# Performance work log

Measured on AMD Instinct MI355X. Metric: run time of the kernel, lower is better.

The kernel has to match this reference:

```python
import jax, jax.numpy as jnp
import numpy as np

HIDDEN = 2048
GAMMA = 0.96875
SCALE_BASE = 512  # XPOS default from torchscale / Jamie-Stirling/RetNet


def _xpos(x, downscale=False):
    # x: [B, L, d]. Faithful port of XPOS with offset=0.
    B, L, d = x.shape
    half = d // 2
    # per-dim scale vector: (arange(0,d,2) + 0.4d) / (1.4d)
    scale_vec = (jnp.arange(0, d, 2, dtype=jnp.float32) + 0.4 * d) / (1.4 * d)  # [half]
    power = jnp.arange(L, dtype=jnp.float32) / SCALE_BASE                        # [L]
    scale = scale_vec[None, :] ** power[:, None]                                 # [L, half]
    # fixed_pos_embedding over `half` frequency dims
    inv_freq = 1.0 / (10000.0 ** (jnp.arange(half, dtype=jnp.float32) / half))   # [half]
    sinusoid = jnp.arange(L, dtype=jnp.float32)[:, None] * inv_freq[None, :]     # [L, half]
    sin, cos = jnp.sin(sinusoid), jnp.cos(sinusoid)
    if downscale:
        scale = 1.0 / scale
    # duplicate_interleave: [L, half] -> [L, d] with each column repeated twice
    sin_s = jnp.repeat(sin * scale, 2, axis=-1)  # [L, d]
    cos_s = jnp.repeat(cos * scale, 2, axis=-1)  # [L, d]
    # rotate_every_two
    x1 = x[..., 0::2]
    x2 = x[..., 1::2]
    rot = jnp.stack((-x2, x1), axis=-1).reshape(x.shape)
    return x * cos_s[None] + rot * sin_s[None]


def _decay_matrix(L):
    n = jnp.arange(L)[:, None]
    m = jnp.arange(L)[None, :]
    mask = n >= m
    # clamp exponent to avoid overflow where masked (torch sets NaN->0)
    D = jnp.where(mask, GAMMA ** jnp.maximum(n - m, 0).astype(jnp.float32), 0.0)
    return D  # [L, L]


def setup_inputs() -> dict:
    key = jax.random.key(0)
    kx, kq, kk, kv = jax.random.split(key, 4)
    B, S, H = 4, 2048, HIDDEN
    X = jax.random.normal(kx, (B, S, H), dtype=jnp.float32)
    W_Q = jax.random.normal(kq, (H, H), dtype=jnp.float32) / H
    W_K = jax.random.normal(kk, (H, H), dtype=jnp.float32) / H
    W_V = jax.random.normal(kv, (H, H), dtype=jnp.float32) / H
    return {"X": X, "W_Q": W_Q, "W_K": W_K, "W_V": W_V}


def reference(X, W_Q, W_K, W_V):
    B, S, H = X.shape
    Q = _xpos(X @ W_Q)                   # [B, S, H]
    K = _xpos(X @ W_K, downscale=True)   # [B, S, H]
    V = X @ W_V                          # [B, S, H]
    D = _decay_matrix(S)                 # [S, S]
    att = jnp.einsum("bnh,bmh->bnm", Q, K) * D[None]  # [B, S, S]
    return att @ V                       # [B, S, H]
```

## Files before the change

kernel.cpp:

```cpp
#include <hip/hip_runtime.h>
#include <math.h>


typedef __attribute__((ext_vector_type(8))) short short8;
typedef __attribute__((ext_vector_type(4))) float f32x4;
typedef __attribute__((ext_vector_type(4))) unsigned short us4;

#define BM 128
#define ABAND 384

static __device__ __forceinline__ unsigned short f2bf(float f) {
    unsigned int u = __float_as_uint(f);
    u += 0x7FFFu + ((u >> 16) & 1u);
    return (unsigned short)(u >> 16);
}

static __device__ __forceinline__ void gload16(const unsigned short* g, unsigned short* l) {
    __builtin_amdgcn_global_load_lds(
        (const __attribute__((address_space(1))) unsigned int*)g,
        (__attribute__((address_space(3))) unsigned int*)l, 16, 0, 0);
}

template <int STAGE, int BNt, int BKt>
static __device__ __forceinline__ void gemm_core(
    const unsigned short* __restrict__ A,
    const unsigned short* __restrict__ Bt,
    void* __restrict__ Cv,
    unsigned short* __restrict__ Cq,
    unsigned short* __restrict__ Ck,
    unsigned short* __restrict__ Cvt,
    int lda, int ldb, int Kd,
    long long sA, long long sB, long long sC,
    int bx, int by, int zb,
    unsigned short* As, unsigned short* Bs)
{
    constexpr int S = 2048, H = 2048;
    constexpr int NJ = BNt / 32;
    constexpr int KS = BKt / 32;
    constexpr int CR = BKt / 8;
    constexpr int RG = 64 / CR;
    constexpr int GA = 32 / RG;
    constexpr int GB = (BNt / 4) / RG;

    const int rowBase = by * BM;
    const int colBase = bx * BNt;

    A  += (long long)zb * sA;
    Bt += (long long)zb * sB;

    const int tid  = threadIdx.x;
    const int wave = tid >> 6;
    const int lane = tid & 63;
    const int wm = (wave & 1) * 64;
    const int wn = (wave >> 1) * (BNt / 2);

    f32x4 acc[4][NJ];
#pragma unroll
    for (int i = 0; i < 4; ++i)
#pragma unroll
        for (int j = 0; j < NJ; ++j) acc[i][j] = (f32x4){0.f, 0.f, 0.f, 0.f};

    int kmax = Kd;
    if (STAGE == 4) { int km = rowBase + BM; kmax = km < Kd ? km : Kd; }
    int k0s = 0;
    if (STAGE == 4) {
        int kb0 = 2 * by - 4; k0s = (kb0 > 0 ? kb0 : 0) * 64;
        A -= k0s;
    }

    const int cpos = lane % CR;
    const int rig  = lane / CR;
    const int waveArow = wave * 32;
    const int waveBrow = wave * (BNt / 4);
    unsigned short* lA = As + wave * (32 * BKt);
    unsigned short* lB = Bs + wave * ((BNt / 4) * BKt);

    auto stage_tile = [&](int kb) {
#pragma unroll
        for (int g = 0; g < GA; ++g) {
            int r = waveArow + g * RG + rig;
            gload16(A + (size_t)(rowBase + r) * lda + kb + ((cpos ^ (r & 7)) * 8),
                    lA + g * 512);
        }
#pragma unroll
        for (int g = 0; g < GB; ++g) {
            int r = waveBrow + g * RG + rig;
            gload16(Bt + (size_t)(colBase + r) * ldb + kb + ((cpos ^ (r & 7)) * 8),
                    lB + g * 512);
        }
    };

    stage_tile(k0s);

    const int fr = lane & 15;
    const int qd = lane >> 4;
    const int fsw = fr & 7;

    for (int k0 = k0s; k0 < kmax; k0 += BKt) {
        __syncthreads();
        short8 aF[KS][4], bF[KS][NJ];
#pragma unroll
        for (int kk = 0; kk < KS; ++kk) {
#pragma unroll
            for (int i = 0; i < 4; ++i)
                aF[kk][i] = *(const short8*)&As[(wm + i * 16 + fr) * BKt + (((kk * 4 + qd) ^ fsw) * 8)];
#pragma unroll
            for (int j = 0; j < NJ; ++j)
                bF[kk][j] = *(const short8*)&Bs[(wn + j * 16 + fr) * BKt + (((kk * 4 + qd) ^ fsw) * 8)];
        }
        __syncthreads();
        if (k0 + BKt < kmax) stage_tile(k0 + BKt);
#pragma unroll
        for (int kk = 0; kk < KS; ++kk)
#pragma unroll
            for (int i = 0; i < 4; ++i)
#pragma unroll
                for (int j = 0; j < NJ; ++j)
                    acc[i][j] = __builtin_amdgcn_mfma_f32_16x16x32_bf16(aF[kk][i], bF[kk][j], acc[i][j], 0, 0, 0);
    }

    if (STAGE == 1) {
        const int mode = colBase >> 11;
        if (mode < 2) {
            unsigned short* Co = (mode == 0) ? Cq : Ck;
            const float psgn = (mode == 1) ? -1.953125e-3f : 1.953125e-3f;
#pragma unroll
            for (int j = 0; j < NJ; ++j) {
                int gc = (colBase & 2047) + wn + j * 16 + fr;
                float c0 = (float)(gc & ~1);
                float l2sv = log2f((c0 + 819.2f) * (1.0f / 2867.2f)) * psgn;
                float invf = exp2f(c0 * -0.0064881407f);
                float s1, c1;
                sincosf(invf, &s1, &c1);
#pragma unroll
                for (int i = 0; i < 4; ++i) {
                    int gr0 = rowBase + wm + i * 16 + qd * 4;
                    float fn = (float)(gr0 & (S - 1));
                    float sN, cN;
                    sincosf(fn * invf, &sN, &cN);
#pragma unroll
                    for (int r = 0; r < 4; ++r) {
                        float scale = exp2f(fn * l2sv);
                        float cs = cN * scale, ss = sN * scale;
                        float v = acc[i][j][r];
                        float o = __shfl_xor(v, 1);
                        float res = (gc & 1) ? fmaf(v, cs, o * ss) : fmaf(v, cs, -o * ss);
                        Co[(size_t)(gr0 + r) * H + gc] = f2bf(res);
                        float sn2 = sN * c1 + cN * s1;
                        cN = cN * c1 - sN * s1;
                        sN = sn2;
                        fn += 1.0f;
                    }
                }
            }
        } else {
#pragma unroll
            for (int j = 0; j < NJ; ++j) {
                int gh = (colBase & 2047) + wn + j * 16 + fr;
#pragma unroll
                for (int i = 0; i < 4; ++i) {
                    int gm0 = rowBase + wm + i * 16 + qd * 4;
                    us4 p;
#pragma unroll
                    for (int r = 0; r < 4; ++r) p[r] = f2bf(acc[i][j][r]);
                    *(us4*)&Cvt[(size_t)gh * 8192 + gm0] = p;
                }
            }
        }
    } else if (STAGE == 3) {
        unsigned short* att = (unsigned short*)Cv + (long long)zb * sC;
        const int kb0 = (2 * by - 4) > 0 ? (2 * by - 4) : 0;
        const int mshift = kb0 * 64;
#pragma unroll
        for (int j = 0; j < NJ; ++j) {
            int m = colBase + wn + j * 16 + fr;
#pragma unroll
            for (int i = 0; i < 4; ++i) {
                int n0 = rowBase + wm + i * 16 + qd * 4;
#pragma unroll
                for (int r = 0; r < 4; ++r) {
                    int d = n0 + r - m;
                    float v = (d >= 0) ? acc[i][j][r] * exp2f((float)d * -0.045803598f) : 0.0f;
                    att[(size_t)(n0 + r) * ABAND + (m - mshift)] = f2bf(v);
                }
            }
        }
    } else {
        float* Co = (float*)Cv + (long long)zb * sC;
#pragma unroll
        for (int j = 0; j < NJ; ++j) {
            int gh = colBase + wn + j * 16 + fr;
#pragma unroll
            for (int i = 0; i < 4; ++i) {
                int gn0 = rowBase + wm + i * 16 + qd * 4;
#pragma unroll
                for (int r = 0; r < 4; ++r)
                    Co[(size_t)(gn0 + r) * H + gh] = acc[i][j][r];
            }
        }
    }
}

template <int STAGE, int BNt, int BKt>
__global__ __launch_bounds__(256)
void gemm_bt(const unsigned short* __restrict__ A,
             const unsigned short* __restrict__ Bt,
             void* __restrict__ Cv,
             unsigned short* __restrict__ Cq,
             unsigned short* __restrict__ Ck,
             unsigned short* __restrict__ Cvt,
             int lda, int ldb, int Kd,
             long long sA, long long sB, long long sC)
{
    __shared__ unsigned short As[BM * BKt];
    __shared__ unsigned short Bs[BNt * BKt];
    int bx, by, zb;
    if (STAGE == 4) {
        int id = blockIdx.x;
        int swz = (id & 7) * 128 + (id >> 3);
        bx = swz >> 6;
        int r = swz & 63;
        zb = r >> 4;
        by = 15 - (r & 15);
    } else {
        bx = blockIdx.x; by = blockIdx.y; zb = 0;
    }
    gemm_core<STAGE, BNt, BKt>(A, Bt, Cv, Cq, Ck, Cvt, lda, ldb, Kd,
                               sA, sB, sC, bx, by, zb, As, Bs);
}

__global__ __launch_bounds__(256)
void fused_vatt(const unsigned short* __restrict__ Xb,
                const unsigned short* __restrict__ Wt,
                const unsigned short* __restrict__ Qb,
                const unsigned short* __restrict__ Kb,
                unsigned short* __restrict__ att,
                unsigned short* __restrict__ Vt)
{
    constexpr int S = 2048, H = 2048;
    constexpr long long SH = (long long)S * H;
    constexpr long long SB = (long long)S * ABAND;
    __shared__ unsigned short smem[16384];
    if (blockIdx.x < 360) {
        int t = blockIdx.x;
        int swz = (t & 7) * 45 + (t >> 3);
        int zb = swz / 90;
        int tt = swz - zb * 90;
        int bx, by;
        if (tt < 6) {
            by = (tt < 2) ? 0 : 1;
            bx = tt - ((by == 0) ? 0 : 2);
        } else {
            by = 2 + (tt - 6) / 6;
            int kb0 = 2 * by - 4;
            bx = (kb0 > 0 ? kb0 : 0) + (tt - 6) % 6;
        }
        gemm_core<3, 64, 64>(Qb, Kb, att, nullptr, nullptr, nullptr,
                             H, H, H, SH, SH, SB, bx, by, zb,
                             smem, smem + 8192);
    } else {
        int id = blockIdx.x - 360;
        int bx = 32 + (id & 15);
        int by = id >> 4;
        gemm_core<1, 128, 64>(Xb, Wt, nullptr, nullptr, nullptr, Vt,
                              H, H, H, 0, 0, 0, bx, by, 0,
                              smem, smem + 8192);
    }
}

__global__ __launch_bounds__(256)
void cvt_fused(const float* __restrict__ X, unsigned short* __restrict__ Xb,
               const float* __restrict__ W0, const float* __restrict__ W1,
               const float* __restrict__ W2, unsigned short* __restrict__ Wt) {
    __shared__ float t[64][65];
    if (blockIdx.x < 3072) {
        int id = blockIdx.x;
        int z = id >> 10, rem = id & 1023;
        const float* W = (z == 0) ? W0 : (z == 1) ? W1 : W2;
        unsigned short* Wo = Wt + (size_t)z * 4194304;
        int bx = (rem & 31) * 64, by = (rem >> 5) * 64;
        int tx = threadIdx.x & 63, ty = threadIdx.x >> 6;
#pragma unroll
        for (int r = 0; r < 64; r += 4)
            t[ty + r][tx] = W[(size_t)(by + ty + r) * 2048 + bx + tx];
        __syncthreads();
#pragma unroll
        for (int r = 0; r < 64; r += 4)
            Wo[(size_t)(bx + ty + r) * 2048 + by + tx] = f2bf(t[tx][ty + r]);
    } else {
        int id = blockIdx.x - 3072;
        const float4* X4 = (const float4*)X;
        short8* O8 = (short8*)Xb;
#pragma unroll
        for (int c = 0; c < 4; ++c) {
            size_t u = (size_t)c * (2048 * 256) + (size_t)id * 256 + threadIdx.x;
            float4 a = X4[u * 2];
            float4 b = X4[u * 2 + 1];
            short8 o;
            o[0] = f2bf(a.x); o[1] = f2bf(a.y); o[2] = f2bf(a.z); o[3] = f2bf(a.w);
            o[4] = f2bf(b.x); o[5] = f2bf(b.y); o[6] = f2bf(b.z); o[7] = f2bf(b.w);
            O8[u] = o;
        }
    }
}

extern "C" void kernel_launch(void* const* d_in, const int* in_sizes, int n_in,
                              void* d_out, int out_size, void* d_ws, size_t ws_size,
                              hipStream_t stream) {
    const int S = 2048, H = 2048;
    const long long MH = 16777216;
    const long long HH = 4194304;
    const long long SH = (long long)S * H;
    const long long SB = (long long)S * ABAND;

    const float* X  = (const float*)d_in[0];
    const float* WQ = (const float*)d_in[1];
    const float* WK = (const float*)d_in[2];
    const float* WV = (const float*)d_in[3];
    float* out = (float*)d_out;

    unsigned short* Xb    = (unsigned short*)d_ws;
    unsigned short* WtAll = Xb + MH;
    unsigned short* Qb    = WtAll + 3 * HH;
    unsigned short* Kb    = Qb + MH;
    unsigned short* Vt    = Kb + MH;
    unsigned short* att   = Vt + MH;

    cvt_fused<<<5120, 256, 0, stream>>>(X, Xb, WQ, WK, WV, WtAll);

    gemm_bt<1, 128, 64><<<dim3(32, 64), 256, 0, stream>>>(Xb, WtAll, nullptr, Qb, Kb, Vt,
                                                          H, H, H, 0, 0, 0);
    fused_vatt<<<1384, 256, 0, stream>>>(Xb, WtAll, Qb, Kb, att, Vt);

    gemm_bt<4, 128, 64><<<1024, 256, 0, stream>>>(att, Vt, out, nullptr, nullptr, nullptr,
                                                  ABAND, 8192, S, SB, 2048, SH);
}
```

Before: 422.0 us.

## Replace Q/K projection GEMM with 256x256 8-wave ping-pong pipelined kernel

Adds a dedicated Q/K projection kernel that uses 256x256 tiles, 512 threads and double-buffered LDS. Each k-step is split into four MFMA phases interleaved with async global-to-LDS prefetch, explicit vmcnt waits, barriers and setprio. The XPOS epilogue moves into this kernel, and the generic stage-1 path keeps only the V-transpose output. The aim is more data reuse per tile and better overlap of loads with MFMA. In exchange it uses 128KB of LDS, carries high register pressure from 32 accumulators, and depends on fragile hand-written wait counts.

Result: slower. 473.7 us (+12.2%).

```diff
diff --git a/kernel.cpp b/kernel.cpp
--- a/kernel.cpp
+++ b/kernel.cpp
@@ -19,6 +19,206 @@
     __builtin_amdgcn_global_load_lds(
         (const __attribute__((address_space(1))) unsigned int*)g,
         (__attribute__((address_space(3))) unsigned int*)l, 16, 0, 0);
+}
+
+#define MFMA __builtin_amdgcn_mfma_f32_16x16x32_bf16
+
+__global__ __launch_bounds__(512, 2)
+void qk_8phase(const unsigned short* __restrict__ A,
+               const unsigned short* __restrict__ Bt,
+               unsigned short* __restrict__ Cq,
+               unsigned short* __restrict__ Ck)
+{
+    constexpr int S = 2048, H = 2048, NT = 2048 / 64;
+    const int rowBase = blockIdx.y * 256;
+    const int colBase = blockIdx.x * 256;
+
+    __shared__ unsigned short As[32768];
+    __shared__ unsigned short Bs[32768];
+
+    const int tid  = threadIdx.x;
+    const int wave = tid >> 6;
+    const int lane = tid & 63;
+    const int wm = (wave >> 2) * 128;
+    const int wn = (wave & 3) * 64;
+
+    const int row8 = lane >> 3;
+    const int csw  = ((lane & 7) ^ row8) * 8;
+
+    f32x4 acc[8][4];
+#pragma unroll
+    for (int i = 0; i < 8; ++i)
+#pragma unroll
+        for (int j = 0; j < 4; ++j) acc[i][j] = (f32x4){0.f, 0.f, 0.f, 0.f};
+
+    auto stgA = [&](int t1, int b1, int u) {
+#pragma unroll
+        for (int g = 0; g < 2; ++g) {
+            int s0 = g * 64 + wave * 8;
+            int R0 = (s0 < 64 ? s0 : s0 + 64) + u * 64;
+            gload16(A + (size_t)(rowBase + R0 + row8) * H + t1 * 64 + csw,
+                    As + b1 * 16384 + R0 * 64);
+        }
+    };
+    auto stgB = [&](int t1, int b1, int q) {
+#pragma unroll
+        for (int g = 0; g < 2; ++g) {
+            int s0 = g * 64 + wave * 8;
+            int R0 = ((s0 >> 5) << 6) + q * 32 + (s0 & 31);
+            gload16(Bt + (size_t)(colBase + R0 + row8) * H + t1 * 64 + csw,
+                    Bs + b1 * 16384 + R0 * 64);
+        }
+    };
+
+    stgA(0, 0, 0); stgB(0, 0, 0); stgB(0, 0, 1); stgA(0, 0, 1);
+    __builtin_amdgcn_sched_barrier(0);
+    asm volatile("s_waitcnt vmcnt(4)" ::: "memory");
+    __builtin_amdgcn_sched_barrier(0);
+    __builtin_amdgcn_s_barrier();
+    asm volatile("" ::: "memory");
+
+    const int fr  = lane & 15;
+    const int qd  = lane >> 4;
+    const int fsw = fr & 7;
+    const int c0  = (qd ^ fsw) * 8;
+    const int c1  = ((4 + qd) ^ fsw) * 8;
+    const int aRow = wm + fr;
+    const int bRow = wn + fr;
+
+    for (int t = 0; t < NT; ++t) {
+        const int b = t & 1;
+        const unsigned short* Ab = As + b * 16384;
+        const unsigned short* Bb = Bs + b * 16384;
+        const bool pf = (t + 1 < NT);
+        short8 aF[4][2], bF[2][2], bG[2][2];
+
+#pragma unroll
+        for (int i = 0; i < 4; ++i) {
+            aF[i][0] = *(const short8*)&Ab[(aRow + i * 16) * 64 + c0];
+            aF[i][1] = *(const short8*)&Ab[(aRow + i * 16) * 64 + c1];
+        }
+#pragma unroll
+        for (int j = 0; j < 2; ++j) {
+            bF[j][0] = *(const short8*)&Bb[(bRow + j * 16) * 64 + c0];
+            bF[j][1] = *(const short8*)&Bb[(bRow + j * 16) * 64 + c1];
+        }
+        __builtin_amdgcn_sched_barrier(0);
+        asm volatile("s_waitcnt vmcnt(2)" ::: "memory");
+        __builtin_amdgcn_sched_barrier(0);
+        __builtin_amdgcn_s_barrier();
+        __builtin_amdgcn_s_setprio(1);
+#pragma unroll
+        for (int i = 0; i < 4; ++i)
+#pragma unroll
+            for (int j = 0; j < 2; ++j) {
+                acc[i][j] = MFMA(aF[i][0], bF[j][0], acc[i][j], 0, 0, 0);
+                acc[i][j] = MFMA(aF[i][1], bF[j][1], acc[i][j], 0, 0, 0);
+            }
+        __builtin_amdgcn_s_setprio(0);
+        __builtin_amdgcn_s_barrier();
+
+#pragma unroll
+        for (int j = 0; j < 2; ++j) {
+            bG[j][0] = *(const short8*)&Bb[(bRow + 32 + j * 16) * 64 + c0];
+            bG[j][1] = *(const short8*)&Bb[(bRow + 32 + j * 16) * 64 + c1];
+        }
+        if (pf) { stgA(t + 1, b ^ 1, 0); stgB(t + 1, b ^ 1, 0); }
+        __builtin_amdgcn_sched_barrier(0);
+        if (pf) { asm volatile("s_waitcnt vmcnt(4)" ::: "memory"); }
+        else    { asm volatile("s_waitcnt vmcnt(0)" ::: "memory"); }
+        __builtin_amdgcn_sched_barrier(0);
+        __builtin_amdgcn_s_barrier();
+        __builtin_amdgcn_s_setprio(1);
+#pragma unroll
+        for (int i = 0; i < 4; ++i)
+#pragma unroll
+            for (int j = 0; j < 2; ++j) {
+                acc[i][j + 2] = MFMA(aF[i][0], bG[j][0], acc[i][j + 2], 0, 0, 0);
+                acc[i][j + 2] = MFMA(aF[i][1], bG[j][1], acc[i][j + 2], 0, 0, 0);
+            }
+        __builtin_amdgcn_s_setprio(0);
+        __builtin_amdgcn_s_barrier();
+
+#pragma unroll
+        for (int i = 0; i < 4; ++i) {
+            aF[i][0] = *(const short8*)&Ab[(aRow + 64 + i * 16) * 64 + c0];
+            aF[i][1] = *(const short8*)&Ab[(aRow + 64 + i * 16) * 64 + c1];
+        }
+#pragma unroll
+        for (int j = 0; j < 2; ++j) {
+            bF[j][0] = *(const short8*)&Bb[(bRow + j * 16) * 64 + c0];
+            bF[j][1] = *(const short8*)&Bb[(bRow + j * 16) * 64 + c1];
+        }
+        if (pf) stgB(t + 1, b ^ 1, 1);
+        __builtin_amdgcn_sched_barrier(0);
+        __builtin_amdgcn_s_barrier();
+        __builtin_amdgcn_s_setprio(1);
+#pragma unroll
+        for (int i = 0; i < 4; ++i)
+#pragma unroll
+            for (int j = 0; j < 2; ++j) {
+                acc[i + 4][j] = MFMA(aF[i][0], bF[j][0], acc[i + 4][j], 0, 0, 0);
+                acc[i + 4][j] = MFMA(aF[i][1], bF[j][1], acc[i + 4][j], 0, 0, 0);
+            }
+        __builtin_amdgcn_s_setprio(0);
+        __builtin_amdgcn_s_barrier();
+
+#pragma unroll
+        for (int j = 0; j < 2; ++j) {
+            bG[j][0] = *(const short8*)&Bb[(bRow + 32 + j * 16) * 64 + c0];
+            bG[j][1] = *(const short8*)&Bb[(bRow + 32 + j * 16) * 64 + c1];
+        }
+        if (pf) stgA(t + 1, b ^ 1, 1);
+        __builtin_amdgcn_sched_barrier(0);
+        if (pf) { asm volatile("s_waitcnt vmcnt(4)" ::: "memory"); }
+        else    { asm volatile("s_waitcnt vmcnt(0)" ::: "memory"); }
+        __builtin_amdgcn_sched_barrier(0);
+        __builtin_amdgcn_s_barrier();
+        __builtin_amdgcn_s_setprio(1);
+#pragma unroll
+        for (int i = 0; i < 4; ++i)
+#pragma unroll
+            for (int j = 0; j < 2; ++j) {
+                acc[i + 4][j + 2] = MFMA(aF[i][0], bG[j][0], acc[i + 4][j + 2], 0, 0, 0);
+                acc[i + 4][j + 2] = MFMA(aF[i][1], bG[j][1], acc[i + 4][j + 2], 0, 0, 0);
+            }
+        __builtin_amdgcn_s_setprio(0);
+        __builtin_amdgcn_s_barrier();
+        asm volatile("" ::: "memory");
+    }
+
+    const int mode = colBase >> 11;
+    unsigned short* Co = (mode == 0) ? Cq : Ck;
+    const float psgn = (mode == 1) ? -1.953125e-3f : 1.953125e-3f;
+#pragma unroll
+    for (int j = 0; j < 4; ++j) {
+        int gc = (colBase & 2047) + wn + j * 16 + fr;
+        float c0f = (float)(gc & ~1);
+        float l2sv = log2f((c0f + 819.2f) * (1.0f / 2867.2f)) * psgn;
+        float invf = exp2f(c0f * -0.0064881407f);
+        float s1, c1f;
+        sincosf(invf, &s1, &c1f);
+#pragma unroll
+        for (int i = 0; i < 8; ++i) {
+            int gr0 = rowBase + wm + i * 16 + qd * 4;
+            float fn = (float)(gr0 & (S - 1));
+            float sN, cN;
+            sincosf(fn * invf, &sN, &cN);
+#pragma unroll
+            for (int r = 0; r < 4; ++r) {
+                float scale = exp2f(fn * l2sv);
+                float cs = cN * scale, ss = sN * scale;
+                float v = acc[i][j][r];
+                float o = __shfl_xor(v, 1);
+                float res = (gc & 1) ? fmaf(v, cs, o * ss) : fmaf(v, cs, -o * ss);
+                Co[(size_t)(gr0 + r) * H + gc] = f2bf(res);
+                float sn2 = sN * c1f + cN * s1;
+                cN = cN * c1f - sN * s1;
+                sN = sn2;
+                fn += 1.0f;
+            }
+        }
+    }
 }
 
 template <int STAGE, int BNt, int BKt>
@@ -26,8 +226,6 @@
     const unsigned short* __restrict__ A,
     const unsigned short* __restrict__ Bt,
     void* __restrict__ Cv,
-    unsigned short* __restrict__ Cq,
-    unsigned short* __restrict__ Ck,
     unsigned short* __restrict__ Cvt,
     int lda, int ldb, int Kd,
     long long sA, long long sB, long long sC,
@@ -116,55 +314,20 @@
             for (int i = 0; i < 4; ++i)
 #pragma unroll
                 for (int j = 0; j < NJ; ++j)
-                    acc[i][j] = __builtin_amdgcn_mfma_f32_16x16x32_bf16(aF[kk][i], bF[kk][j], acc[i][j], 0, 0, 0);
+                    acc[i][j] = MFMA(aF[kk][i], bF[kk][j], acc[i][j], 0, 0, 0);
     }
 
     if (STAGE == 1) {
-        const int mode = colBase >> 11;
-        if (mode < 2) {
-            unsigned short* Co = (mode == 0) ? Cq : Ck;
-            const float psgn = (mode == 1) ? -1.953125e-3f : 1.953125e-3f;
-#pragma unroll
-            for (int j = 0; j < NJ; ++j) {
-                int gc = (colBase & 2047) + wn + j * 16 + fr;
-                float c0 = (float)(gc & ~1);
-                float l2sv = log2f((c0 + 819.2f) * (1.0f / 2867.2f)) * psgn;
-                float invf = exp2f(c0 * -0.0064881407f);
-                float s1, c1;
-                sincosf(invf, &s1, &c1);
-#pragma unroll
-                for (int i = 0; i < 4; ++i) {
-                    int gr0 = rowBase + wm + i * 16 + qd * 4;
-                    float fn = (float)(gr0 & (S - 1));
-                    float sN, cN;
-                    sincosf(fn * invf, &sN, &cN);
-#pragma unroll
-                    for (int r = 0; r < 4; ++r) {
-                        float scale = exp2f(fn * l2sv);
-                        float cs = cN * scale, ss = sN * scale;
-                        float v = acc[i][j][r];
-                        float o = __shfl_xor(v, 1);
-                        float res = (gc & 1) ? fmaf(v, cs, o * ss) : fmaf(v, cs, -o * ss);
-                        Co[(size_t)(gr0 + r) * H + gc] = f2bf(res);
-                        float sn2 = sN * c1 + cN * s1;
-                        cN = cN * c1 - sN * s1;
-                        sN = sn2;
-                        fn += 1.0f;
-                    }
-                }
-            }
-        } else {
-#pragma unroll
-            for (int j = 0; j < NJ; ++j) {
-                int gh = (colBase & 2047) + wn + j * 16 + fr;
-#pragma unroll
-                for (int i = 0; i < 4; ++i) {
-                    int gm0 = rowBase + wm + i * 16 + qd * 4;
-                    us4 p;
-#pragma unroll
-                    for (int r = 0; r < 4; ++r) p[r] = f2bf(acc[i][j][r]);
-                    *(us4*)&Cvt[(size_t)gh * 8192 + gm0] = p;
-                }
+#pragma unroll
+        for (int j = 0; j < NJ; ++j) {
+            int gh = (colBase & 2047) + wn + j * 16 + fr;
+#pragma unroll
+            for (int i = 0; i < 4; ++i) {
+                int gm0 = rowBase + wm + i * 16 + qd * 4;
+                us4 p;
+#pragma unroll
+                for (int r = 0; r < 4; ++r) p[r] = f2bf(acc[i][j][r]);
+                *(us4*)&Cvt[(size_t)gh * 8192 + gm0] = p;
             }
         }
     } else if (STAGE == 3) {
@@ -206,8 +369,6 @@
 void gemm_bt(const unsigned short* __restrict__ A,
              const unsigned short* __restrict__ Bt,
              void* __restrict__ Cv,
-             unsigned short* __restrict__ Cq,
-             unsigned short* __restrict__ Ck,
              unsigned short* __restrict__ Cvt,
              int lda, int ldb, int Kd,
              long long sA, long long sB, long long sC)
@@ -225,7 +386,7 @@
     } else {
         bx = blockIdx.x; by = blockIdx.y; zb = 0;
     }
-    gemm_core<STAGE, BNt, BKt>(A, Bt, Cv, Cq, Ck, Cvt, lda, ldb, Kd,
+    gemm_core<STAGE, BNt, BKt>(A, Bt, Cv, Cvt, lda, ldb, Kd,
                                sA, sB, sC, bx, by, zb, As, Bs);
 }
 
@@ -255,14 +416,14 @@
             int kb0 = 2 * by - 4;
             bx = (kb0 > 0 ? kb0 : 0) + (tt - 6) % 6;
         }
-        gemm_core<3, 64, 64>(Qb, Kb, att, nullptr, nullptr, nullptr,
+        gemm_core<3, 64, 64>(Qb, Kb, att, nullptr,
                              H, H, H, SH, SH, SB, bx, by, zb,
                              smem, smem + 8192);
     } else {
         int id = blockIdx.x - 360;
         int bx = 32 + (id & 15);
         int by = id >> 4;
-        gemm_core<1, 128, 64>(Xb, Wt, nullptr, nullptr, nullptr, Vt,
+        gemm_core<1, 128, 64>(Xb, Wt, nullptr, Vt,
                               H, H, H, 0, 0, 0, bx, by, 0,
                               smem, smem + 8192);
     }
@@ -328,10 +489,10 @@
 
     cvt_fused<<<5120, 256, 0, stream>>>(X, Xb, WQ, WK, WV, WtAll);
 
-    gemm_bt<1, 128, 64><<<dim3(32, 64), 256, 0, stream>>>(Xb, WtAll, nullptr, Qb, Kb, Vt,
-                                                          H, H, H, 0, 0, 0);
+    qk_8phase<<<dim3(16, 32), 512, 0, stream>>>(Xb, WtAll, Qb, Kb);
+
     fused_vatt<<<1384, 256, 0, stream>>>(Xb, WtAll, Qb, Kb, att, Vt);
 
-    gemm_bt<4, 128, 64><<<1024, 256, 0, stream>>>(att, Vt, out, nullptr, nullptr, nullptr,
+    gemm_bt<4, 128, 64><<<1024, 256, 0, stream>>>(att, Vt, out, nullptr,
                                                   ABAND, 8192, S, SB, 2048, SH);
 }
```
